# Kernel optimization log

Hardware: AMD Instinct MI355X
Metric: run time of the kernel (lower is better)

Reference implementation:

```python
import jax, jax.numpy as jnp
import numpy as np

IN_FEATURES = 4096
OUT_FEATURES = 11008
BLOCK_SIZE = 64
BITS = 4
RANGE_MAX = 2 ** (BITS - 1) - 1  # 7


def setup_inputs() -> dict:
    key = jax.random.key(0)
    k1, k2, k3, k4 = jax.random.split(key, 4)
    n_blocks = OUT_FEATURES * IN_FEATURES // BLOCK_SIZE
    x = jax.random.normal(k1, (4, 2048, IN_FEATURES), dtype=jnp.float32)
    # int4 codes in [-7, 7]; stored signed int. Use randint in [-7, 8).
    weight_quant = jax.random.randint(k2, (n_blocks, BLOCK_SIZE), -RANGE_MAX, RANGE_MAX + 1, dtype=jnp.int32)
    weight_absmax = jax.random.uniform(k3, (n_blocks, 1), dtype=jnp.float32, minval=1e-5, maxval=1.0)
    bias = jax.random.normal(k4, (OUT_FEATURES,), dtype=jnp.float32)
    return {"x": x, "weight_quant": weight_quant, "weight_absmax": weight_absmax, "bias": bias}


def reference(x, weight_quant, weight_absmax, bias):
    # Blockwise dequant: q/range_max * absmax per block, reshape to (out, in). padding=0.
    w = (weight_quant.astype(jnp.float32) / RANGE_MAX) * weight_absmax  # [n_blocks, block]
    w = w.reshape(OUT_FEATURES, IN_FEATURES)
    # F.linear: y = x @ W^T + b
    return jnp.einsum('bsi,oi->bso', x, w) + bias
```

## Files before the change

### kernel.cpp

```cpp
#include <hip/hip_runtime.h>


#define K_DIM 4096
#define N_DIM 11008
#define M_DIM 8192
#define NT_K 64
#define AB_OFF 98304

typedef _Float16 f16;
typedef _Float16 f16x8 __attribute__((ext_vector_type(8)));
typedef float f32x16 __attribute__((ext_vector_type(16)));
typedef float fv4 __attribute__((ext_vector_type(4)));
typedef int iv4 __attribute__((ext_vector_type(4)));

__device__ __forceinline__ void gload16(const void* g, void* lds) {
  __builtin_amdgcn_global_load_lds(
      (__attribute__((address_space(1))) void*)g,
      (__attribute__((address_space(3))) void*)lds,
      16, 0, 0);
}

__global__ __launch_bounds__(256) void prep_kernel(const float* __restrict__ x,
                                                   f16* __restrict__ xo, int n8x,
                                                   const int* __restrict__ q,
                                                   const float* __restrict__ amax,
                                                   f16* __restrict__ wo, int n8w) {
  int i = blockIdx.x * blockDim.x + threadIdx.x;
  if (i < n8x) {
    const fv4* xv = (const fv4*)x;
    fv4 a = __builtin_nontemporal_load(xv + 2 * (size_t)i);
    fv4 b = __builtin_nontemporal_load(xv + 2 * (size_t)i + 1);
    f16x8 o;
    o[0] = (f16)a.x; o[1] = (f16)a.y; o[2] = (f16)a.z; o[3] = (f16)a.w;
    o[4] = (f16)b.x; o[5] = (f16)b.y; o[6] = (f16)b.z; o[7] = (f16)b.w;
    *(f16x8*)(xo + (size_t)i * 8) = o;
  } else {
    int j = i - n8x;
    if (j >= n8w) return;
    const iv4* qv = (const iv4*)q;
    iv4 a = __builtin_nontemporal_load(qv + 2 * (size_t)j);
    iv4 b = __builtin_nontemporal_load(qv + 2 * (size_t)j + 1);
    float s = amax[j >> 3] * (1.0f / 7.0f);
    f16x8 o;
    o[0] = (f16)((float)a.x * s); o[1] = (f16)((float)a.y * s);
    o[2] = (f16)((float)a.z * s); o[3] = (f16)((float)a.w * s);
    o[4] = (f16)((float)b.x * s); o[5] = (f16)((float)b.y * s);
    o[6] = (f16)((float)b.z * s); o[7] = (f16)((float)b.w * s);
    *(f16x8*)(wo + (size_t)j * 8) = o;
  }
}

__global__ __launch_bounds__(512, 2) void gemm_f16_bt(const f16* __restrict__ A,
                                                      const f16* __restrict__ B,
                                                      const float* __restrict__ bias,
                                                      float* __restrict__ C) {
  __shared__ __align__(16) char lds[163840];

  const int tid = threadIdx.x;
  const int w = tid >> 6;
  const int l = tid & 63;
  const int wr = w >> 2;
  const int wc = w & 3;

  const int wg = blockIdx.x;
  const int swz = (wg & 7) * 172 + (wg >> 3);
  const int mt = swz / 43;
  const int nt = swz % 43;
  const int m0 = mt * 256;
  const int n0 = nt * 256;

  const int l31 = l & 31;
  const int lbase = (l31 >> 1) << 7;
  const int lxor = ((l31 >> 1) & 7) << 4;
  const int lk0 = ((l & 1) << 6) | ((l >> 5) << 4);
  const int lt0 = lk0 ^ lxor;
  const int lt1 = (lk0 | 32) ^ lxor;

  const char* AsrcP[2];
  const char* BsrcP[2];
#pragma unroll
  for (int j = 0; j < 2; ++j) {
    const int u = ((w + j * 8) << 10) + l * 16;
    const int r = u >> 7;
    const int cp = (u & 127) ^ ((r & 7) << 4);
    const int ra = 2 * r + (cp >> 6);
    const int kb = cp & 63;
    AsrcP[j] = (const char*)A + (size_t)(m0 + ra) * (K_DIM * 2) + kb;
    BsrcP[j] = (const char*)B + (size_t)(n0 + ra) * (K_DIM * 2) + kb;
  }

  char* ldsc = (char*)lds;

#define STAGE_A(dst_off, koff)              \
  {                                         \
    char* d_ = ldsc + (dst_off) + w * 1024; \
    gload16(AsrcP[0] + (koff), d_);         \
    gload16(AsrcP[1] + (koff), d_ + 8192);  \
  }
#define STAGE_B(dst_off, koff)              \
  {                                         \
    char* d_ = ldsc + (dst_off) + w * 1024; \
    gload16(BsrcP[0] + (koff), d_);         \
    gload16(BsrcP[1] + (koff), d_ + 8192);  \
  }

  f32x16 acc[4][2];
#pragma unroll
  for (int i = 0; i < 4; ++i)
#pragma unroll
    for (int j = 0; j < 2; ++j) acc[i][j] = (f32x16)0.f;

  const int aW = wr * 8192;
  const int bW = wc * 4096;

  STAGE_A(0, 0);
  STAGE_A(16384, 64);
  STAGE_B(AB_OFF, 0);
  STAGE_B(AB_OFF + 16384, 64);
  STAGE_A(32768, 128);
  STAGE_A(32768 + 16384, 192);
  STAGE_B(AB_OFF + 32768, 128);
  asm volatile("s_waitcnt vmcnt(6)" ::: "memory");
  __builtin_amdgcn_s_barrier();

  int ap = 0;
  int ap2 = 65536;

  for (int t = 0; t < NT_K; ++t) {
    const int p = t & 1;
    const int pn = p ^ 1;
    const int Bb = AB_OFF + p * 32768;
    const int Bn = AB_OFF + pn * 32768;
    const int t1 = (t + 1 < NT_K) ? (t + 1) : (NT_K - 1);
    const int t2 = (t + 2 < NT_K) ? (t + 2) : (NT_K - 1);
    const int k1 = t1 * 128;
    const int k2 = t2 * 128;

#pragma unroll
    for (int pi = 0; pi < 4; ++pi) {
      const int kk = pi >> 1;
      const int kt = (pi & 1) ? lt1 : lt0;

      f16x8 af[4], bf[2];
#pragma unroll
      for (int mf = 0; mf < 4; ++mf)
        af[mf] = *(const f16x8*)(ldsc + ap + kk * 16384 + aW + mf * 2048 + lbase + kt);
#pragma unroll
      for (int nf = 0; nf < 2; ++nf)
        bf[nf] = *(const f16x8*)(ldsc + Bb + kk * 16384 + bW + nf * 2048 + lbase + kt);

      if (pi == 0) {
        STAGE_B(Bn + 16384, k1 + 64);
      } else if (pi == 1) {
        STAGE_A(ap2, k2);
      } else if (pi == 2) {
        STAGE_A(ap2 + 16384, k2 + 64);
      } else {
        STAGE_B(Bb, k2);
      }

      __builtin_amdgcn_s_barrier();
      asm volatile("s_waitcnt lgkmcnt(0)" ::: "memory");
      __builtin_amdgcn_sched_barrier(0);
      __builtin_amdgcn_s_setprio(1);
#pragma unroll
      for (int mf = 0; mf < 4; ++mf)
#pragma unroll
        for (int nf = 0; nf < 2; ++nf)
          acc[mf][nf] = __builtin_amdgcn_mfma_f32_32x32x16_f16(af[mf], bf[nf], acc[mf][nf], 0, 0, 0);
      __builtin_amdgcn_s_setprio(0);
      if (pi == 3) asm volatile("s_waitcnt vmcnt(6)" ::: "memory");
      __builtin_amdgcn_s_barrier();
    }

    ap += 32768;  if (ap == AB_OFF) ap = 0;
    ap2 += 32768; if (ap2 == AB_OFF) ap2 = 0;
  }

  const int rbase = 4 * (l >> 5);
  float bv[2];
#pragma unroll
  for (int nf = 0; nf < 2; ++nf) bv[nf] = bias[n0 + wc * 64 + nf * 32 + l31];
#pragma unroll
  for (int mf = 0; mf < 4; ++mf) {
#pragma unroll
    for (int nf = 0; nf < 2; ++nf) {
      const size_t col = n0 + wc * 64 + nf * 32 + l31;
#pragma unroll
      for (int q = 0; q < 4; ++q) {
#pragma unroll
        for (int j = 0; j < 4; ++j) {
          const int row = m0 + wr * 128 + mf * 32 + rbase + 8 * q + j;
          __builtin_nontemporal_store(acc[mf][nf][q * 4 + j] + bv[nf],
                                      &C[(size_t)row * N_DIM + col]);
        }
      }
    }
  }
#undef STAGE_A
#undef STAGE_B
}

extern "C" void kernel_launch(void* const* d_in, const int* in_sizes, int n_in,
                              void* d_out, int out_size, void* d_ws, size_t ws_size,
                              hipStream_t stream) {
  const float* x = (const float*)d_in[0];
  const int* wq = (const int*)d_in[1];
  const float* amax = (const float*)d_in[2];
  const float* bias = (const float*)d_in[3];
  float* out = (float*)d_out;

  f16* Xh = (f16*)d_ws;
  f16* Wh = (f16*)((char*)d_ws + (size_t)M_DIM * K_DIM * 2);

  {
    int n8x = M_DIM * K_DIM / 8;
    int n8w = N_DIM * K_DIM / 8;
    int nthr = n8x + n8w;
    prep_kernel<<<(nthr + 255) / 256, 256, 0, stream>>>(x, Xh, n8x, wq, amax, Wh, n8w);
  }
  {
    dim3 grid((M_DIM / 256) * (N_DIM / 256));
    gemm_f16_bt<<<grid, 512, 0, stream>>>(Xh, Wh, bias, out);
  }
}
```

Before: 855.6 us.

## Pre-tile fp16 operands in MFMA fragment order for contiguous LDS staging

The prep kernel now writes X and dequantized W in a tiled layout, per 256-row tile and 64-wide K step, arranged so each lane's 16-byte fragment sits contiguously. The GEMM then stages contiguous 1KB chunks per wave and reads LDS with a simple lane-linear offset, dropping the XOR swizzle and strided global row addressing. The aim is fully coalesced global loads and conflict-free LDS reads. The cost is strided, less coalesced reads in the prep kernel, and LDS reads now depend on the linear layout being bank-conflict free.

```diff
diff --git a/kernel.cpp b/kernel.cpp
--- a/kernel.cpp
+++ b/kernel.cpp
@@ -6,6 +6,7 @@
 #define M_DIM 8192
 #define NT_K 64
 #define AB_OFF 98304
+#define TILE_BYTES 2097152
 
 typedef _Float16 f16;
 typedef _Float16 f16x8 __attribute__((ext_vector_type(8)));
@@ -21,26 +22,41 @@
 }
 
 __global__ __launch_bounds__(256) void prep_kernel(const float* __restrict__ x,
-                                                   f16* __restrict__ xo, int n8x,
+                                                   f16* __restrict__ xo, int n16x,
                                                    const int* __restrict__ q,
                                                    const float* __restrict__ amax,
-                                                   f16* __restrict__ wo, int n8w) {
+                                                   f16* __restrict__ wo, int n16w) {
   int i = blockIdx.x * blockDim.x + threadIdx.x;
-  if (i < n8x) {
-    const fv4* xv = (const fv4*)x;
-    fv4 a = __builtin_nontemporal_load(xv + 2 * (size_t)i);
-    fv4 b = __builtin_nontemporal_load(xv + 2 * (size_t)i + 1);
+  if (i < n16x) {
+    const int lam = i & 63;
+    const int F = (i >> 6) & 15;
+    const int kk = (i >> 10) & 1;
+    const int t = (i >> 11) & 63;
+    const int mt = i >> 17;
+    const int row = mt * 256 + ((F >> 1) << 5) + (lam & 31);
+    const int kc = t * 64 + (kk << 5) + ((F & 1) << 4) + ((lam >> 5) << 3);
+    const fv4* src = (const fv4*)(x + (size_t)row * K_DIM + kc);
+    fv4 a = __builtin_nontemporal_load(src);
+    fv4 b = __builtin_nontemporal_load(src + 1);
     f16x8 o;
     o[0] = (f16)a.x; o[1] = (f16)a.y; o[2] = (f16)a.z; o[3] = (f16)a.w;
     o[4] = (f16)b.x; o[5] = (f16)b.y; o[6] = (f16)b.z; o[7] = (f16)b.w;
     *(f16x8*)(xo + (size_t)i * 8) = o;
   } else {
-    int j = i - n8x;
-    if (j >= n8w) return;
-    const iv4* qv = (const iv4*)q;
-    iv4 a = __builtin_nontemporal_load(qv + 2 * (size_t)j);
-    iv4 b = __builtin_nontemporal_load(qv + 2 * (size_t)j + 1);
-    float s = amax[j >> 3] * (1.0f / 7.0f);
+    int j = i - n16x;
+    if (j >= n16w) return;
+    const int lam = j & 63;
+    const int F = (j >> 6) & 15;
+    const int kk = (j >> 10) & 1;
+    const int t = (j >> 11) & 63;
+    const int nt = j >> 17;
+    const int row = nt * 256 + ((F >> 1) << 5) + (lam & 31);
+    const int kc = t * 64 + (kk << 5) + ((F & 1) << 4) + ((lam >> 5) << 3);
+    const size_t base = (size_t)row * K_DIM + kc;
+    const iv4* src = (const iv4*)(q + base);
+    iv4 a = __builtin_nontemporal_load(src);
+    iv4 b = __builtin_nontemporal_load(src + 1);
+    float s = amax[base >> 6] * (1.0f / 7.0f);
     f16x8 o;
     o[0] = (f16)((float)a.x * s); o[1] = (f16)((float)a.y * s);
     o[2] = (f16)((float)a.z * s); o[3] = (f16)((float)a.w * s);
@@ -69,39 +85,22 @@
   const int m0 = mt * 256;
   const int n0 = nt * 256;
 
-  const int l31 = l & 31;
-  const int lbase = (l31 >> 1) << 7;
-  const int lxor = ((l31 >> 1) & 7) << 4;
-  const int lk0 = ((l & 1) << 6) | ((l >> 5) << 4);
-  const int lt0 = lk0 ^ lxor;
-  const int lt1 = (lk0 | 32) ^ lxor;
-
-  const char* AsrcP[2];
-  const char* BsrcP[2];
-#pragma unroll
-  for (int j = 0; j < 2; ++j) {
-    const int u = ((w + j * 8) << 10) + l * 16;
-    const int r = u >> 7;
-    const int cp = (u & 127) ^ ((r & 7) << 4);
-    const int ra = 2 * r + (cp >> 6);
-    const int kb = cp & 63;
-    AsrcP[j] = (const char*)A + (size_t)(m0 + ra) * (K_DIM * 2) + kb;
-    BsrcP[j] = (const char*)B + (size_t)(n0 + ra) * (K_DIM * 2) + kb;
-  }
+  const char* Abase = (const char*)A + (size_t)mt * TILE_BYTES + (w << 10) + (l << 4);
+  const char* Bbase = (const char*)B + (size_t)nt * TILE_BYTES + (w << 10) + (l << 4);
 
   char* ldsc = (char*)lds;
 
-#define STAGE_A(dst_off, koff)              \
-  {                                         \
-    char* d_ = ldsc + (dst_off) + w * 1024; \
-    gload16(AsrcP[0] + (koff), d_);         \
-    gload16(AsrcP[1] + (koff), d_ + 8192);  \
-  }
-#define STAGE_B(dst_off, koff)              \
-  {                                         \
-    char* d_ = ldsc + (dst_off) + w * 1024; \
-    gload16(BsrcP[0] + (koff), d_);         \
-    gload16(BsrcP[1] + (koff), d_ + 8192);  \
+#define STAGE_A(dst_off, koff)               \
+  {                                          \
+    char* d_ = ldsc + (dst_off) + (w << 10); \
+    gload16(Abase + (koff), d_);             \
+    gload16(Abase + (koff) + 8192, d_ + 8192); \
+  }
+#define STAGE_B(dst_off, koff)               \
+  {                                          \
+    char* d_ = ldsc + (dst_off) + (w << 10); \
+    gload16(Bbase + (koff), d_);             \
+    gload16(Bbase + (koff) + 8192, d_ + 8192); \
   }
 
   f32x16 acc[4][2];
@@ -110,16 +109,17 @@
 #pragma unroll
     for (int j = 0; j < 2; ++j) acc[i][j] = (f32x16)0.f;
 
-  const int aW = wr * 8192;
-  const int bW = wc * 4096;
+  const int l16 = l << 4;
+  const int aF0 = (wr << 3) << 10;
+  const int bF0 = (wc << 2) << 10;
 
   STAGE_A(0, 0);
-  STAGE_A(16384, 64);
+  STAGE_A(16384, 16384);
   STAGE_B(AB_OFF, 0);
-  STAGE_B(AB_OFF + 16384, 64);
-  STAGE_A(32768, 128);
-  STAGE_A(32768 + 16384, 192);
-  STAGE_B(AB_OFF + 32768, 128);
+  STAGE_B(AB_OFF + 16384, 16384);
+  STAGE_A(32768, 32768);
+  STAGE_A(32768 + 16384, 32768 + 16384);
+  STAGE_B(AB_OFF + 32768, 32768);
   asm volatile("s_waitcnt vmcnt(6)" ::: "memory");
   __builtin_amdgcn_s_barrier();
 
@@ -133,28 +133,28 @@
     const int Bn = AB_OFF + pn * 32768;
     const int t1 = (t + 1 < NT_K) ? (t + 1) : (NT_K - 1);
     const int t2 = (t + 2 < NT_K) ? (t + 2) : (NT_K - 1);
-    const int k1 = t1 * 128;
-    const int k2 = t2 * 128;
+    const int k1 = t1 * 32768;
+    const int k2 = t2 * 32768;
 
 #pragma unroll
     for (int pi = 0; pi < 4; ++pi) {
       const int kk = pi >> 1;
-      const int kt = (pi & 1) ? lt1 : lt0;
+      const int ks = pi & 1;
 
       f16x8 af[4], bf[2];
 #pragma unroll
       for (int mf = 0; mf < 4; ++mf)
-        af[mf] = *(const f16x8*)(ldsc + ap + kk * 16384 + aW + mf * 2048 + lbase + kt);
+        af[mf] = *(const f16x8*)(ldsc + ap + kk * 16384 + aF0 + ((mf << 1) | ks) * 1024 + l16);
 #pragma unroll
       for (int nf = 0; nf < 2; ++nf)
-        bf[nf] = *(const f16x8*)(ldsc + Bb + kk * 16384 + bW + nf * 2048 + lbase + kt);
+        bf[nf] = *(const f16x8*)(ldsc + Bb + kk * 16384 + bF0 + ((nf << 1) | ks) * 1024 + l16);
 
       if (pi == 0) {
-        STAGE_B(Bn + 16384, k1 + 64);
+        STAGE_B(Bn + 16384, k1 + 16384);
       } else if (pi == 1) {
         STAGE_A(ap2, k2);
       } else if (pi == 2) {
-        STAGE_A(ap2 + 16384, k2 + 64);
+        STAGE_A(ap2 + 16384, k2 + 16384);
       } else {
         STAGE_B(Bb, k2);
       }
@@ -177,6 +177,7 @@
     ap2 += 32768; if (ap2 == AB_OFF) ap2 = 0;
   }
 
+  const int l31 = l & 31;
   const int rbase = 4 * (l >> 5);
   float bv[2];
 #pragma unroll
@@ -187,11 +188,11 @@
     for (int nf = 0; nf < 2; ++nf) {
       const size_t col = n0 + wc * 64 + nf * 32 + l31;
 #pragma unroll
-      for (int q = 0; q < 4; ++q) {
+      for (int qd = 0; qd < 4; ++qd) {
 #pragma unroll
         for (int j = 0; j < 4; ++j) {
-          const int row = m0 + wr * 128 + mf * 32 + rbase + 8 * q + j;
-          __builtin_nontemporal_store(acc[mf][nf][q * 4 + j] + bv[nf],
+          const int row = m0 + wr * 128 + mf * 32 + rbase + 8 * qd + j;
+          __builtin_nontemporal_store(acc[mf][nf][qd * 4 + j] + bv[nf],
                                       &C[(size_t)row * N_DIM + col]);
         }
       }
@@ -214,10 +215,10 @@
   f16* Wh = (f16*)((char*)d_ws + (size_t)M_DIM * K_DIM * 2);
 
   {
-    int n8x = M_DIM * K_DIM / 8;
-    int n8w = N_DIM * K_DIM / 8;
-    int nthr = n8x + n8w;
-    prep_kernel<<<(nthr + 255) / 256, 256, 0, stream>>>(x, Xh, n8x, wq, amax, Wh, n8w);
+    int n16x = M_DIM * K_DIM / 8;
+    int n16w = N_DIM * K_DIM / 8;
+    int nthr = n16x + n16w;
+    prep_kernel<<<(nthr + 255) / 256, 256, 0, stream>>>(x, Xh, n16x, wq, amax, Wh, n16w);
   }
   {
     dim3 grid((M_DIM / 256) * (N_DIM / 256));
```

Result: slower. 883.9 us (+3.3%).
